# Performance work log

Measured on AMD Instinct MI355X. Metric: run time of the kernel, lower is better.

## Reference

```python
import jax, jax.numpy as jnp
import numpy as np

HEADS = 20  # SDXL-style: hidden_size 1280 / head_dim 64
IP_SCALE = 1.0


def setup_inputs() -> dict:
    key = jax.random.key(0)
    ks = jax.random.split(key, 12)
    B, Sq, T, C, D, NIP = 4, 4096, 77, 1280, 2048, 16
    s = lambda fan: 1.0 / np.sqrt(fan)
    # post-softmax multiplicative mask: col 0 (sot token) forced to 1, rest a binary spatial mask
    spat = (jax.random.uniform(ks[0], (1, Sq, 1)) < 0.5).astype(jnp.float32)
    attention_mask = jnp.concatenate([jnp.ones((1, Sq, 1)), jnp.tile(spat, (1, 1, T - 1))], axis=-1)
    return {
        "hidden_states": jax.random.normal(ks[1], (B, Sq, C), jnp.float32),
        "encoder_hidden_states": jax.random.normal(ks[2], (B, T, D), jnp.float32),
        "ip_hidden_states": jax.random.normal(ks[3], (B, NIP, D), jnp.float32),
        "attention_mask": attention_mask,
        "Wq": jax.random.normal(ks[4], (C, C), jnp.float32) * s(C),
        "Wk": jax.random.normal(ks[5], (D, C), jnp.float32) * s(D),
        "Wv": jax.random.normal(ks[6], (D, C), jnp.float32) * s(D),
        "Wo": jax.random.normal(ks[7], (C, C), jnp.float32) * s(C),
        "bo": jnp.zeros((C,), jnp.float32),
        "Wk_ip": jax.random.normal(ks[8], (D, C), jnp.float32) * s(D),
        "Wv_ip": jax.random.normal(ks[9], (D, C), jnp.float32) * s(D),
    }


def reference(hidden_states, encoder_hidden_states, ip_hidden_states, attention_mask,
              Wq, Wk, Wv, Wo, bo, Wk_ip, Wv_ip):
    B, Sq, C = hidden_states.shape
    H = HEADS
    d = C // H
    scale = d ** -0.5
    # projections (torch Linear with weights stored [in, out])
    q = (hidden_states @ Wq).reshape(B, Sq, H, d)
    k = (encoder_hidden_states @ Wk).reshape(B, -1, H, d)
    v = (encoder_hidden_states @ Wv).reshape(B, -1, H, d)
    # explicit QK^T softmax, then POST-softmax multiplicative mask (as in get_attention_scores + mask multiply)
    scores = jnp.einsum('bqhd,bkhd->bhqk', q, k) * scale
    probs = jax.nn.softmax(scores, axis=-1)
    probs = probs * attention_mask[:, None, :, :]  # [1,1,Sq,T] broadcast over batch*heads
    out = jnp.einsum('bhqk,bkhd->bqhd', probs, v).reshape(B, Sq, C)
    out = out @ Wo + bo  # to_out[0]; to_out[1] is dropout (identity at eval)
    # IP-adapter stream (single stream, no spatial ip mask): standard SDPA against ip tokens
    k_ip = (ip_hidden_states @ Wk_ip).reshape(B, -1, H, d)
    v_ip = (ip_hidden_states @ Wv_ip).reshape(B, -1, H, d)
    s_ip = jnp.einsum('bqhd,bkhd->bhqk', q, k_ip) * scale
    p_ip = jax.nn.softmax(s_ip, axis=-1)
    ip_out = jnp.einsum('bhqk,bkhd->bqhd', p_ip, v_ip).reshape(B, Sq, C)
    return out + IP_SCALE * ip_out
```

## Files before the change

kernel.cpp:

```cpp
#include <hip/hip_runtime.h>

typedef __attribute__((ext_vector_type(4))) float f32x4;
typedef __attribute__((ext_vector_type(8))) short s16x8;
typedef __attribute__((ext_vector_type(8))) __bf16 bf16x8;
typedef unsigned short u16;

__device__ __forceinline__ u16 f2b(float f) {
  union { float f; unsigned u; } x; x.f = f;
  unsigned r = x.u + 0x7fffu + ((x.u >> 16) & 1u);
  return (u16)(r >> 16);
}
__device__ __forceinline__ float b2f(u16 u) {
  union { unsigned u; float f; } x; x.u = ((unsigned)u) << 16;
  return x.f;
}
__device__ __forceinline__ void gld16(const void* g, void* l) {
  __builtin_amdgcn_global_load_lds(
      (const __attribute__((address_space(1))) unsigned int*)g,
      (__attribute__((address_space(3))) unsigned int*)l, 16, 0, 0);
}
__device__ __forceinline__ f32x4 mfma_bf16(s16x8 a, s16x8 b, f32x4 c) {
  return __builtin_amdgcn_mfma_f32_16x16x32_bf16(
      __builtin_bit_cast(bf16x8, a), __builtin_bit_cast(bf16x8, b), c, 0, 0, 0);
}

#define BAR() asm volatile("s_barrier" ::: "memory")
#define WAITVM4() asm volatile("s_waitcnt vmcnt(4)" ::: "memory")

__global__ void k_convert_all(const float* __restrict__ hs, const float* __restrict__ ehs,
                              const float* __restrict__ iph,
                              u16* __restrict__ hsb, u16* __restrict__ ehsb,
                              u16* __restrict__ ipb) {
  const int n1 = 16384 * 1280 / 4, n2 = 308 * 2048 / 4, n3 = 64 * 2048 / 4;
  int i = blockIdx.x * blockDim.x + threadIdx.x;
  const float* src; u16* dst; int j = i;
  if (i < n1) { src = hs; dst = hsb; }
  else if (i < n1 + n2) { src = ehs; dst = ehsb; j = i - n1; }
  else if (i < n1 + n2 + n3) { src = iph; dst = ipb; j = i - n1 - n2; }
  else return;
  float4 v = ((const float4*)src)[j];
  ushort4 o;
  o.x = f2b(v.x); o.y = f2b(v.y); o.z = f2b(v.z); o.w = f2b(v.w);
  ((ushort4*)dst)[j] = o;
}

__device__ __forceinline__ void transpose_tile(const float* __restrict__ W,
                                               u16* __restrict__ WT, int K, int N) {
  __shared__ float tile[32][33];
  int n0 = blockIdx.x * 32, k0 = blockIdx.y * 32;
  int tx = threadIdx.x & 31, ty = threadIdx.x >> 5;
#pragma unroll
  for (int i = 0; i < 32; i += 8)
    tile[ty + i][tx] = W[(size_t)(k0 + ty + i) * N + n0 + tx];
  __syncthreads();
#pragma unroll
  for (int i = 0; i < 32; i += 8)
    WT[(size_t)(n0 + ty + i) * K + k0 + tx] = f2b(tile[tx][ty + i]);
}

__global__ void k_transpose4(const float* W0, const float* W1, const float* W2,
                             const float* W3, u16* T0, u16* T1, u16* T2, u16* T3,
                             int K, int N) {
  int z = blockIdx.z;
  const float* W = (z == 0) ? W0 : (z == 1) ? W1 : (z == 2) ? W2 : W3;
  u16* T = (z == 0) ? T0 : (z == 1) ? T1 : (z == 2) ? T2 : T3;
  transpose_tile(W, T, K, N);
}
__global__ void k_transpose2(const float* W0, const float* W1, u16* T0, u16* T1,
                             int K, int N) {
  int z = blockIdx.z;
  transpose_tile(z ? W1 : W0, z ? T1 : T0, K, N);
}

__device__ __forceinline__ void gemm_core0(
    const u16* __restrict__ A, const u16* __restrict__ BT,
    int M, int N, int K, u16* __restrict__ outb, int m0, int n0) {
  const int tid = threadIdx.x;
  const int l = tid & 63;
  const int w = tid >> 6;
  const int wr = w >> 1, wc = w & 1;
  __shared__ u16 As[128 * 32];
  __shared__ u16 Bs[128 * 32];
  f32x4 acc[4][4] = {};

  const int o0 = tid * 16;
  const int o1 = o0 + 4096;
  const int ra0 = o0 >> 6, ca0 = (o0 & 63) >> 1;
  const int ra1 = o1 >> 6, ca1 = (o1 & 63) >> 1;
  int ga0 = m0 + ra0; if (ga0 >= M) ga0 = M - 1;
  int ga1 = m0 + ra1; if (ga1 >= M) ga1 = M - 1;
  const u16* Ar0 = A + (size_t)ga0 * K + ca0;
  const u16* Ar1 = A + (size_t)ga1 * K + ca1;
  const u16* Br0 = BT + (size_t)(n0 + ra0) * K + ca0;
  const u16* Br1 = BT + (size_t)(n0 + ra1) * K + ca1;

  for (int k0 = 0; k0 < K; k0 += 32) {
    gld16(Ar0 + k0, &As[o0 >> 1]);
    gld16(Ar1 + k0, &As[o1 >> 1]);
    gld16(Br0 + k0, &Bs[o0 >> 1]);
    gld16(Br1 + k0, &Bs[o1 >> 1]);
    __syncthreads();
    s16x8 af[4], bfr[4];
#pragma unroll
    for (int mi = 0; mi < 4; ++mi)
      af[mi] = *(const s16x8*)&As[(wr * 64 + mi * 16 + (l & 15)) * 32 + (l >> 4) * 8];
#pragma unroll
    for (int ni = 0; ni < 4; ++ni)
      bfr[ni] = *(const s16x8*)&Bs[(wc * 64 + ni * 16 + (l & 15)) * 32 + (l >> 4) * 8];
#pragma unroll
    for (int mi = 0; mi < 4; ++mi)
#pragma unroll
      for (int ni = 0; ni < 4; ++ni)
        acc[mi][ni] = mfma_bf16(af[mi], bfr[ni], acc[mi][ni]);
    __syncthreads();
  }

#pragma unroll
  for (int mi = 0; mi < 4; ++mi) {
    const int mbase = m0 + wr * 64 + mi * 16 + (l >> 4) * 4;
#pragma unroll
    for (int ni = 0; ni < 4; ++ni) {
      const int ncol = n0 + wc * 64 + ni * 16 + (l & 15);
#pragma unroll
      for (int r = 0; r < 4; ++r) {
        int m = mbase + r;
        if (m < M) outb[(size_t)m * N + ncol] = f2b(acc[mi][ni][r]);
      }
    }
  }
}

__global__ __launch_bounds__(256) void k_gemm_small4(
    const u16* __restrict__ ehsb, const u16* __restrict__ ipb,
    const u16* __restrict__ WkT, const u16* __restrict__ WvT,
    const u16* __restrict__ WkipT, const u16* __restrict__ WvipT,
    u16* kbuf, u16* vbuf, u16* kipb, u16* vipb) {
  const int z = blockIdx.z;
  const int M = (z < 2) ? 308 : 64;
  const int m0 = blockIdx.y * 128;
  if (m0 >= M) return;
  const u16* A = (z < 2) ? ehsb : ipb;
  const u16* BT = (z == 0) ? WkT : (z == 1) ? WvT : (z == 2) ? WkipT : WvipT;
  u16* out = (z == 0) ? kbuf : (z == 1) ? vbuf : (z == 2) ? kipb : vipb;
  gemm_core0(A, BT, M, 1280, 2048, out, m0, blockIdx.x * 128);
}

template <int EPI>
__global__ __launch_bounds__(512, 2) void k_gemm256(
    const u16* __restrict__ A, const u16* __restrict__ BT,
    int N, int K, float alpha,
    u16* __restrict__ outb, float* __restrict__ outf,
    const float* __restrict__ bias, const u16* __restrict__ ipadd,
    int nbx) {
  __shared__ u16 lds[65536];
  const int tid = threadIdx.x, l = tid & 63, w = tid >> 6;
  const int lr = l & 15, lg = l >> 4;
  const int wr = w >> 2, wc = w & 3;

  const int nwg = gridDim.x;
  const int q = nwg >> 3, r = nwg & 7;
  const int xcd = blockIdx.x & 7, lid = blockIdx.x >> 3;
  const int wg = (xcd < r) ? (xcd * (q + 1) + lid)
                           : (r * (q + 1) + (xcd - r) * q + lid);
  const int bm0 = (wg / nbx) * 256, bn0 = (wg % nbx) * 256;

  const int c0 = tid, c1 = tid + 512;
  const int row0 = c0 >> 2, row1 = c1 >> 2;
  const int sp0 = ((c0 & 3) ^ ((row0 >> 1) & 3)) * 8;
  const int sp1 = ((c1 & 3) ^ ((row1 >> 1) & 3)) * 8;
  const size_t aO0 = (size_t)(bm0 + row0) * K + sp0;
  const size_t aO1 = (size_t)(bm0 + row1) * K + sp1;
  const size_t bO0 = (size_t)(bn0 + row0) * K + sp0;
  const size_t bO1 = (size_t)(bn0 + row1) * K + sp1;
  const int d0 = c0 * 8, d1 = c1 * 8;

  const int KT = K >> 6;
  f32x4 acc[8][4] = {};
  s16x8 bfv[4], afv[4];

  const int xsw = (lg ^ ((lr >> 1) & 3)) * 8;
  const int aRow = (wr * 128 + lr) * 32 + xsw;
  const int bRow = 16384 + (wc * 64 + lr) * 32 + xsw;

#define STAGE_A(buf, kk, kt)                                            \
  {                                                                     \
    const int base_ = (buf) * 32768 + (kk) * 8192;                      \
    const size_t go_ = (size_t)(kt) * 64 + (kk) * 32;                   \
    gld16(A + aO0 + go_, &lds[base_ + d0]);                             \
    gld16(A + aO1 + go_, &lds[base_ + d1]);                             \
  }
#define STAGE_B(buf, kk, kt)                                            \
  {                                                                     \
    const int base_ = (buf) * 32768 + 16384 + (kk) * 8192;              \
    const size_t go_ = (size_t)(kt) * 64 + (kk) * 32;                   \
    gld16(BT + bO0 + go_, &lds[base_ + d0]);                            \
    gld16(BT + bO1 + go_, &lds[base_ + d1]);                            \
  }

  STAGE_A(0, 0, 0);
  STAGE_B(0, 0, 0);
  STAGE_A(0, 1, 0);
  STAGE_B(0, 1, 0);
  WAITVM4();
  BAR();

  int cur = 0;
  for (int j = 0; j < KT; ++j) {
    const int nx = cur ^ 1;
    const int cb = cur * 32768;
    const bool pf = (j + 1 < KT);
#pragma unroll
    for (int ni = 0; ni < 4; ++ni)
      bfv[ni] = *(const s16x8*)&lds[cb + bRow + ni * 512];
#pragma unroll
    for (int mi = 0; mi < 4; ++mi)
      afv[mi] = *(const s16x8*)&lds[cb + aRow + mi * 512];
    if (pf) STAGE_A(nx, 0, j + 1);
    __builtin_amdgcn_s_setprio(1);
#pragma unroll
    for (int mi = 0; mi < 4; ++mi)
#pragma unroll
      for (int ni = 0; ni < 4; ++ni)
        acc[mi][ni] = mfma_bf16(afv[mi], bfv[ni], acc[mi][ni]);
    __builtin_amdgcn_s_setprio(0);
    BAR();
#pragma unroll
    for (int mi = 0; mi < 4; ++mi)
      afv[mi] = *(const s16x8*)&lds[cb + aRow + (mi + 4) * 512];
    if (pf) STAGE_B(nx, 0, j + 1);
    __builtin_amdgcn_s_setprio(1);
#pragma unroll
    for (int mi = 0; mi < 4; ++mi)
#pragma unroll
      for (int ni = 0; ni < 4; ++ni)
        acc[mi + 4][ni] = mfma_bf16(afv[mi], bfv[ni], acc[mi + 4][ni]);
    __builtin_amdgcn_s_setprio(0);
    WAITVM4();
    BAR();
#pragma unroll
    for (int ni = 0; ni < 4; ++ni)
      bfv[ni] = *(const s16x8*)&lds[cb + 8192 + bRow + ni * 512];
#pragma unroll
    for (int mi = 0; mi < 4; ++mi)
      afv[mi] = *(const s16x8*)&lds[cb + 8192 + aRow + mi * 512];
    if (pf) STAGE_A(nx, 1, j + 1);
    __builtin_amdgcn_s_setprio(1);
#pragma unroll
    for (int mi = 0; mi < 4; ++mi)
#pragma unroll
      for (int ni = 0; ni < 4; ++ni)
        acc[mi][ni] = mfma_bf16(afv[mi], bfv[ni], acc[mi][ni]);
    __builtin_amdgcn_s_setprio(0);
    BAR();
#pragma unroll
    for (int mi = 0; mi < 4; ++mi)
      afv[mi] = *(const s16x8*)&lds[cb + 8192 + aRow + (mi + 4) * 512];
    if (pf) STAGE_B(nx, 1, j + 1);
    __builtin_amdgcn_s_setprio(1);
#pragma unroll
    for (int mi = 0; mi < 4; ++mi)
#pragma unroll
      for (int ni = 0; ni < 4; ++ni)
        acc[mi + 4][ni] = mfma_bf16(afv[mi], bfv[ni], acc[mi + 4][ni]);
    __builtin_amdgcn_s_setprio(0);
    WAITVM4();
    BAR();
    cur = nx;
  }

  asm volatile("s_waitcnt vmcnt(0)" ::: "memory");
  __syncthreads();

  if constexpr (EPI == 0) {
#pragma unroll
    for (int half = 0; half < 2; ++half) {
      if (half) __syncthreads();
      if (wr == half) {
#pragma unroll
        for (int mi = 0; mi < 8; ++mi) {
          const int row = mi * 16 + lg * 4;
#pragma unroll
          for (int ni = 0; ni < 4; ++ni) {
            const int col = wc * 64 + ni * 16 + lr;
#pragma unroll
            for (int rr = 0; rr < 4; ++rr)
              lds[(row + rr) * 256 + col] = f2b(acc[mi][ni][rr] * alpha);
          }
        }
      }
      __syncthreads();
      for (int s = tid; s < 4096; s += 512) {
        const int row = s >> 5, ch = s & 31;
        *(int4*)(outb + (size_t)(bm0 + half * 128 + row) * N + bn0 + ch * 8) =
            *(const int4*)&lds[row * 256 + ch * 8];
      }
    }
  } else {
#pragma unroll
    for (int mi = 0; mi < 8; ++mi) {
      const int mrow = bm0 + wr * 128 + mi * 16 + lg * 4;
#pragma unroll
      for (int ni = 0; ni < 4; ++ni) {
        const int ncol = bn0 + wc * 64 + ni * 16 + lr;
#pragma unroll
        for (int rr = 0; rr < 4; ++rr) {
          const size_t idx = (size_t)(mrow + rr) * N + ncol;
          outf[idx] = acc[mi][ni][rr] + bias[ncol] + b2f(ipadd[idx]);
        }
      }
    }
  }
#undef STAGE_A
#undef STAGE_B
}

__global__ __launch_bounds__(512, 4) void k_attn(
    const u16* __restrict__ Q,
    const u16* __restrict__ Kb,
    const u16* __restrict__ Vb,
    const u16* __restrict__ Kip,
    const u16* __restrict__ Vip,
    const float* __restrict__ mask,
    u16* __restrict__ Oattn,
    u16* __restrict__ Oip) {
  const int qt = blockIdx.x, h = blockIdx.y, b = blockIdx.z;
  const int tid = threadIdx.x, l = tid & 63, w = tid >> 6;
  const int lr = l & 15, lg = l >> 4;
  const int r0 = w * 16;
  const int m0 = b * 4096 + qt * 128;

  __shared__ u16 KV[192][72];
  __shared__ u16 Ps[128][104];
  __shared__ u16 P2s[128][40];

  const u16* qrow = Q + (size_t)(m0 + r0 + lr) * 1280 + h * 64;
  s16x8 aq0 = *(const s16x8*)(qrow + lg * 8);
  s16x8 aq1 = *(const s16x8*)(qrow + 32 + lg * 8);

  for (int s = tid; s < 192 * 8; s += 512) {
    const int row = s >> 3, seg = s & 7;
    int4 v = {0, 0, 0, 0};
    const u16* src = nullptr;
    if (row < 77)       src = Kb  + (size_t)(b * 77 + row) * 1280 + h * 64 + seg * 8;
    else if (row < 80)  src = nullptr;
    else if (row < 96)  src = Kip + (size_t)(b * 16 + row - 80) * 1280 + h * 64 + seg * 8;
    else if (row < 173) src = Vb  + (size_t)(b * 77 + row - 96) * 1280 + h * 64 + seg * 8;
    else if (row < 176) src = nullptr;
    else                src = Vip + (size_t)(b * 16 + row - 176) * 1280 + h * 64 + seg * 8;
    if (src) v = *(const int4*)src;
    *(int4*)&KV[row][(seg ^ ((row >> 3) & 3)) * 8] = v;
  }
  __syncthreads();

  f32x4 sc[5];
  f32x4 sip = {};
#pragma unroll
  for (int t5 = 0; t5 < 6; ++t5) {
    const int trow = t5 * 16 + lr;
    const int qz = (trow >> 3) & 3;
    s16x8 b0 = *(const s16x8*)&KV[trow][(lg ^ qz) * 8];
    s16x8 b1 = *(const s16x8*)&KV[trow][((lg + 4) ^ qz) * 8];
    f32x4 c = {};
    c = mfma_bf16(aq0, b0, c);
    c = mfma_bf16(aq1, b1, c);
    if (t5 < 5) sc[t5] = c; else sip = c;
  }

#pragma unroll
  for (int r = 0; r < 4; ++r) {
    float mx = fmaxf(fmaxf(fmaxf(sc[0][r], sc[1][r]), fmaxf(sc[2][r], sc[3][r])), sc[4][r]);
    mx = fmaxf(mx, __shfl_xor(mx, 1));
    mx = fmaxf(mx, __shfl_xor(mx, 2));
    mx = fmaxf(mx, __shfl_xor(mx, 4));
    mx = fmaxf(mx, __shfl_xor(mx, 8));
    float p[5], sm = 0.f;
#pragma unroll
    for (int t5 = 0; t5 < 5; ++t5) {
      bool valid = (t5 < 4) | (lr < 13);
      p[t5] = valid ? __expf(sc[t5][r] - mx) : 0.f;
      sm += p[t5];
    }
    sm += __shfl_xor(sm, 1);
    sm += __shfl_xor(sm, 2);
    sm += __shfl_xor(sm, 4);
    sm += __shfl_xor(sm, 8);
    const float inv = 1.0f / sm;
    const int row = r0 + lg * 4 + r;
    const int qg = qt * 128 + row;
#pragma unroll
    for (int t5 = 0; t5 < 5; ++t5) {
      int t = t5 * 16 + lr;
      float pf = 0.f;
      if (t < 77) pf = p[t5] * inv * mask[qg * 77 + t];
      Ps[row][t] = f2b(pf);
    }
    Ps[row][80 + lr] = 0;

    float m2 = sip[r];
    m2 = fmaxf(m2, __shfl_xor(m2, 1));
    m2 = fmaxf(m2, __shfl_xor(m2, 2));
    m2 = fmaxf(m2, __shfl_xor(m2, 4));
    m2 = fmaxf(m2, __shfl_xor(m2, 8));
    float pi = __expf(sip[r] - m2);
    float s2 = pi;
    s2 += __shfl_xor(s2, 1);
    s2 += __shfl_xor(s2, 2);
    s2 += __shfl_xor(s2, 4);
    s2 += __shfl_xor(s2, 8);
    P2s[row][lr] = 0;
    P2s[row][16 + lr] = f2b(pi / s2);
  }

  s16x8 ap[3];
#pragma unroll
  for (int ks = 0; ks < 3; ++ks)
    ap[ks] = *(const s16x8*)&Ps[r0 + lr][ks * 32 + lg * 8];
  s16x8 aip = *(const s16x8*)&P2s[r0 + lr][lg * 8];

  f32x4 om[4], oi[4];
#pragma unroll
  for (int nt = 0; nt < 4; ++nt) {
    const int dcol = (nt * 16 + lr) ^ (lg << 3);
    f32x4 o = {};
#pragma unroll
    for (int ks = 0; ks < 3; ++ks) {
      s16x8 bv;
#pragma unroll
      for (int j = 0; j < 8; ++j)
        bv[j] = (short)KV[96 + ks * 32 + lg * 8 + j][dcol];
      o = mfma_bf16(ap[ks], bv, o);
    }
    s16x8 bip;
#pragma unroll
    for (int j = 0; j < 8; ++j)
      bip[j] = (short)KV[160 + lg * 8 + j][dcol];
    f32x4 o2 = {};
    o2 = mfma_bf16(aip, bip, o2);
    om[nt] = o;
    oi[nt] = o2;
  }

  __syncthreads();

  u16 (*Om)[72] = (u16(*)[72]) & KV[0][0];
  u16 (*Oi)[72] = (u16(*)[72]) & Ps[0][0];
#pragma unroll
  for (int nt = 0; nt < 4; ++nt)
#pragma unroll
    for (int r = 0; r < 4; ++r) {
      const int row = r0 + lg * 4 + r;
      const int d = nt * 16 + lr;
      Om[row][d] = f2b(om[nt][r]);
      Oi[row][d] = f2b(oi[nt][r]);
    }
  __syncthreads();

  for (int s = tid; s < 128 * 8; s += 512) {
    const int row = s >> 3, seg = s & 7;
    const size_t g = (size_t)(m0 + row) * 1280 + h * 64 + seg * 8;
    *(int4*)(Oattn + g) = *(const int4*)&Om[row][seg * 8];
    *(int4*)(Oip + g) = *(const int4*)&Oi[row][seg * 8];
  }
}

extern "C" void kernel_launch(void* const* d_in, const int* in_sizes, int n_in,
                              void* d_out, int out_size, void* d_ws, size_t ws_size,
                              hipStream_t stream) {
  (void)in_sizes; (void)n_in; (void)out_size; (void)ws_size;
  const float* hs   = (const float*)d_in[0];
  const float* ehs  = (const float*)d_in[1];
  const float* iph  = (const float*)d_in[2];
  const float* mask = (const float*)d_in[3];
  const float* Wq   = (const float*)d_in[4];
  const float* Wk   = (const float*)d_in[5];
  const float* Wv   = (const float*)d_in[6];
  const float* Wo   = (const float*)d_in[7];
  const float* bo   = (const float*)d_in[8];
  const float* Wkip = (const float*)d_in[9];
  const float* Wvip = (const float*)d_in[10];
  float* out = (float*)d_out;

  char* ws = (char*)d_ws;
  size_t off = 0;
  auto alloc = [&](size_t bytes) {
    char* p = ws + off;
    off += (bytes + 255) & ~(size_t)255;
    return p;
  };
  u16* hsb   = (u16*)alloc(16384ull * 1280 * 2);
  u16* qbuf  = (u16*)alloc(16384ull * 1280 * 2);
  u16* ipout = (u16*)alloc(16384ull * 1280 * 2);
  u16* WqT   = (u16*)alloc(1280ull * 1280 * 2);
  u16* WoT   = (u16*)alloc(1280ull * 1280 * 2);
  u16* WkT   = (u16*)alloc(1280ull * 2048 * 2);
  u16* WvT   = (u16*)alloc(1280ull * 2048 * 2);
  u16* WkipT = (u16*)alloc(1280ull * 2048 * 2);
  u16* WvipT = (u16*)alloc(1280ull * 2048 * 2);
  u16* ehsb  = (u16*)alloc(308ull * 2048 * 2);
  u16* ipb   = (u16*)alloc(64ull * 2048 * 2);
  u16* kbuf  = (u16*)alloc(308ull * 1280 * 2);
  u16* vbuf  = (u16*)alloc(308ull * 1280 * 2);
  u16* kipb  = (u16*)alloc(64ull * 1280 * 2);
  u16* vipb  = (u16*)alloc(64ull * 1280 * 2);

  const int ntot4 = (16384 * 1280 + 308 * 2048 + 64 * 2048) / 4;
  k_convert_all<<<(ntot4 + 255) / 256, 256, 0, stream>>>(hs, ehs, iph, hsb, ehsb, ipb);
  k_transpose4<<<dim3(40, 64, 4), 256, 0, stream>>>(Wk, Wv, Wkip, Wvip,
                                                    WkT, WvT, WkipT, WvipT, 2048, 1280);
  k_transpose2<<<dim3(40, 40, 2), 256, 0, stream>>>(Wq, Wo, WqT, WoT, 1280, 1280);

  k_gemm256<0><<<320, 512, 0, stream>>>(hsb, WqT, 1280, 1280, 0.125f,
                                        qbuf, nullptr, nullptr, nullptr, 5);
  k_gemm_small4<<<dim3(10, 3, 4), 256, 0, stream>>>(ehsb, ipb, WkT, WvT, WkipT, WvipT,
                                                    kbuf, vbuf, kipb, vipb);

  k_attn<<<dim3(32, 20, 4), 512, 0, stream>>>(qbuf, kbuf, vbuf, kipb, vipb, mask,
                                              hsb, ipout);

  k_gemm256<1><<<320, 512, 0, stream>>>(hsb, WoT, 1280, 1280, 1.f,
                                        nullptr, out, bo, ipout, 5);
}
```

Measured before the change: 308.5 us.

## Widen projection GEMM tile to 256x320 so grid fits one wave

Changes the Q and output projection GEMM tile from 256x256 to 256x320, giving 256 workgroups that exactly cover the CUs in a single wave instead of 320 workgroups with a tail. B staging adds a third load issued only by the first four waves, with matching per-wave vmcnt waits. LDS grows to 144 KB and launch bounds drop to one block per CU, trading co-residency latency hiding for removal of wave quantization and higher per-wave MFMA reuse.

```diff
diff --git a/kernel.cpp b/kernel.cpp
--- a/kernel.cpp
+++ b/kernel.cpp
@@ -25,7 +25,6 @@
 }
 
 #define BAR() asm volatile("s_barrier" ::: "memory")
-#define WAITVM4() asm volatile("s_waitcnt vmcnt(4)" ::: "memory")
 
 __global__ void k_convert_all(const float* __restrict__ hs, const float* __restrict__ ehs,
                               const float* __restrict__ iph,
@@ -146,129 +145,137 @@
 }
 
 template <int EPI>
-__global__ __launch_bounds__(512, 2) void k_gemm256(
+__global__ __launch_bounds__(512, 1) void k_gemm256(
     const u16* __restrict__ A, const u16* __restrict__ BT,
     int N, int K, float alpha,
     u16* __restrict__ outb, float* __restrict__ outf,
     const float* __restrict__ bias, const u16* __restrict__ ipadd,
     int nbx) {
-  __shared__ u16 lds[65536];
+  __shared__ u16 lds[73728];
   const int tid = threadIdx.x, l = tid & 63, w = tid >> 6;
   const int lr = l & 15, lg = l >> 4;
   const int wr = w >> 2, wc = w & 3;
+  const bool wlo = (w < 4);
 
   const int nwg = gridDim.x;
   const int q = nwg >> 3, r = nwg & 7;
   const int xcd = blockIdx.x & 7, lid = blockIdx.x >> 3;
   const int wg = (xcd < r) ? (xcd * (q + 1) + lid)
                            : (r * (q + 1) + (xcd - r) * q + lid);
-  const int bm0 = (wg / nbx) * 256, bn0 = (wg % nbx) * 256;
-
-  const int c0 = tid, c1 = tid + 512;
-  const int row0 = c0 >> 2, row1 = c1 >> 2;
-  const int sp0 = ((c0 & 3) ^ ((row0 >> 1) & 3)) * 8;
-  const int sp1 = ((c1 & 3) ^ ((row1 >> 1) & 3)) * 8;
-  const size_t aO0 = (size_t)(bm0 + row0) * K + sp0;
-  const size_t aO1 = (size_t)(bm0 + row1) * K + sp1;
-  const size_t bO0 = (size_t)(bn0 + row0) * K + sp0;
-  const size_t bO1 = (size_t)(bn0 + row1) * K + sp1;
-  const int d0 = c0 * 8, d1 = c1 * 8;
+  const int bm0 = (wg / nbx) * 256, bn0 = (wg % nbx) * 320;
+
+  const int srow = tid >> 2;
+  const int sslot = ((tid & 3) ^ ((srow >> 1) & 3)) * 8;
+  const size_t aO0 = (size_t)(bm0 + srow) * K + sslot;
+  const size_t aO1 = aO0 + (size_t)128 * K;
+  const size_t bO0 = (size_t)(bn0 + srow) * K + sslot;
+  const size_t bO1 = bO0 + (size_t)128 * K;
+  const size_t bO2 = bO0 + (size_t)256 * K;
+  const int d0 = tid * 8, d1 = (tid + 512) * 8, d2 = (tid + 1024) * 8;
 
   const int KT = K >> 6;
-  f32x4 acc[8][4] = {};
-  s16x8 bfv[4], afv[4];
+  f32x4 acc[8][5] = {};
+  s16x8 bfv[5], afv[4];
 
   const int xsw = (lg ^ ((lr >> 1) & 3)) * 8;
   const int aRow = (wr * 128 + lr) * 32 + xsw;
-  const int bRow = 16384 + (wc * 64 + lr) * 32 + xsw;
-
-#define STAGE_A(buf, kk, kt)                                            \
-  {                                                                     \
-    const int base_ = (buf) * 32768 + (kk) * 8192;                      \
-    const size_t go_ = (size_t)(kt) * 64 + (kk) * 32;                   \
-    gld16(A + aO0 + go_, &lds[base_ + d0]);                             \
-    gld16(A + aO1 + go_, &lds[base_ + d1]);                             \
-  }
-#define STAGE_B(buf, kk, kt)                                            \
-  {                                                                     \
-    const int base_ = (buf) * 32768 + 16384 + (kk) * 8192;              \
-    const size_t go_ = (size_t)(kt) * 64 + (kk) * 32;                   \
-    gld16(BT + bO0 + go_, &lds[base_ + d0]);                            \
-    gld16(BT + bO1 + go_, &lds[base_ + d1]);                            \
-  }
+  const int bRow = 32768 + (wc * 80 + lr) * 32 + xsw;
+
+#define STAGE_A(buf, kk, kt)                                           \
+  {                                                                    \
+    const int base_ = (buf) * 16384 + (kk) * 8192;                     \
+    const size_t go_ = (size_t)(kt) * 64 + (kk) * 32;                  \
+    gld16(A + aO0 + go_, &lds[base_ + d0]);                            \
+    gld16(A + aO1 + go_, &lds[base_ + d1]);                            \
+  }
+#define STAGE_B(buf, kk, kt)                                           \
+  {                                                                    \
+    const int base_ = 32768 + (buf) * 20480 + (kk) * 10240;            \
+    const size_t go_ = (size_t)(kt) * 64 + (kk) * 32;                  \
+    gld16(BT + bO0 + go_, &lds[base_ + d0]);                           \
+    gld16(BT + bO1 + go_, &lds[base_ + d1]);                           \
+    if (wlo) gld16(BT + bO2 + go_, &lds[base_ + d2]);                  \
+  }
+#define WAITVM()                                                       \
+  {                                                                    \
+    if (wlo) asm volatile("s_waitcnt vmcnt(5)" ::: "memory");          \
+    else     asm volatile("s_waitcnt vmcnt(4)" ::: "memory");          \
+  }
+#define WAITVM0() asm volatile("s_waitcnt vmcnt(0)" ::: "memory")
 
   STAGE_A(0, 0, 0);
   STAGE_B(0, 0, 0);
   STAGE_A(0, 1, 0);
   STAGE_B(0, 1, 0);
-  WAITVM4();
+  WAITVM();
   BAR();
 
   int cur = 0;
   for (int j = 0; j < KT; ++j) {
     const int nx = cur ^ 1;
-    const int cb = cur * 32768;
+    const int ab = cur * 16384;
+    const int bb = cur * 20480;
     const bool pf = (j + 1 < KT);
 #pragma unroll
-    for (int ni = 0; ni < 4; ++ni)
-      bfv[ni] = *(const s16x8*)&lds[cb + bRow + ni * 512];
-#pragma unroll
-    for (int mi = 0; mi < 4; ++mi)
-      afv[mi] = *(const s16x8*)&lds[cb + aRow + mi * 512];
+    for (int ni = 0; ni < 5; ++ni)
+      bfv[ni] = *(const s16x8*)&lds[bb + bRow + ni * 512];
+#pragma unroll
+    for (int mi = 0; mi < 4; ++mi)
+      afv[mi] = *(const s16x8*)&lds[ab + aRow + mi * 512];
     if (pf) STAGE_A(nx, 0, j + 1);
     __builtin_amdgcn_s_setprio(1);
 #pragma unroll
     for (int mi = 0; mi < 4; ++mi)
 #pragma unroll
-      for (int ni = 0; ni < 4; ++ni)
+      for (int ni = 0; ni < 5; ++ni)
         acc[mi][ni] = mfma_bf16(afv[mi], bfv[ni], acc[mi][ni]);
     __builtin_amdgcn_s_setprio(0);
     BAR();
 #pragma unroll
     for (int mi = 0; mi < 4; ++mi)
-      afv[mi] = *(const s16x8*)&lds[cb + aRow + (mi + 4) * 512];
+      afv[mi] = *(const s16x8*)&lds[ab + aRow + (mi + 4) * 512];
     if (pf) STAGE_B(nx, 0, j + 1);
     __builtin_amdgcn_s_setprio(1);
 #pragma unroll
     for (int mi = 0; mi < 4; ++mi)
 #pragma unroll
-      for (int ni = 0; ni < 4; ++ni)
+      for (int ni = 0; ni < 5; ++ni)
         acc[mi + 4][ni] = mfma_bf16(afv[mi], bfv[ni], acc[mi + 4][ni]);
     __builtin_amdgcn_s_setprio(0);
-    WAITVM4();
+    if (pf) { WAITVM(); } else { WAITVM0(); }
     BAR();
 #pragma unroll
-    for (int ni = 0; ni < 4; ++ni)
-      bfv[ni] = *(const s16x8*)&lds[cb + 8192 + bRow + ni * 512];
-#pragma unroll
-    for (int mi = 0; mi < 4; ++mi)
-      afv[mi] = *(const s16x8*)&lds[cb + 8192 + aRow + mi * 512];
+    for (int ni = 0; ni < 5; ++ni)
+      bfv[ni] = *(const s16x8*)&lds[bb + 10240 + bRow + ni * 512];
+#pragma unroll
+    for (int mi = 0; mi < 4; ++mi)
+      afv[mi] = *(const s16x8*)&lds[ab + 8192 + aRow + mi * 512];
     if (pf) STAGE_A(nx, 1, j + 1);
     __builtin_amdgcn_s_setprio(1);
 #pragma unroll
     for (int mi = 0; mi < 4; ++mi)
 #pragma unroll
-      for (int ni = 0; ni < 4; ++ni)
+      for (int ni = 0; ni < 5; ++ni)
         acc[mi][ni] = mfma_bf16(afv[mi], bfv[ni], acc[mi][ni]);
     __builtin_amdgcn_s_setprio(0);
     BAR();
 #pragma unroll
     for (int mi = 0; mi < 4; ++mi)
-      afv[mi] = *(const s16x8*)&lds[cb + 8192 + aRow + (mi + 4) * 512];
+      afv[mi] = *(const s16x8*)&lds[ab + 8192 + aRow + (mi + 4) * 512];
     if (pf) STAGE_B(nx, 1, j + 1);
     __builtin_amdgcn_s_setprio(1);
 #pragma unroll
     for (int mi = 0; mi < 4; ++mi)
 #pragma unroll
-      for (int ni = 0; ni < 4; ++ni)
+      for (int ni = 0; ni < 5; ++ni)
         acc[mi + 4][ni] = mfma_bf16(afv[mi], bfv[ni], acc[mi + 4][ni]);
     __builtin_amdgcn_s_setprio(0);
-    WAITVM4();
+    if (pf) { WAITVM(); } else { WAITVM0(); }
     BAR();
     cur = nx;
   }
 
-  asm volatile("s_waitcnt vmcnt(0)" ::: "memory");
+  WAITVM0();
   __syncthreads();
 
   if constexpr (EPI == 0) {
@@ -280,19 +287,21 @@
         for (int mi = 0; mi < 8; ++mi) {
           const int row = mi * 16 + lg * 4;
 #pragma unroll
-          for (int ni = 0; ni < 4; ++ni) {
-            const int col = wc * 64 + ni * 16 + lr;
+          for (int ni = 0; ni < 5; ++ni) {
+            const int col = wc * 80 + ni * 16 + lr;
 #pragma unroll
             for (int rr = 0; rr < 4; ++rr)
-              lds[(row + rr) * 256 + col] = f2b(acc[mi][ni][rr] * alpha);
+              lds[(row + rr) * 320 + col] = f2b(acc[mi][ni][rr] * alpha);
           }
         }
       }
       __syncthreads();
-      for (int s = tid; s < 4096; s += 512) {
-        const int row = s >> 5, ch = s & 31;
-        *(int4*)(outb + (size_t)(bm0 + half * 128 + row) * N + bn0 + ch * 8) =
-            *(const int4*)&lds[row * 256 + ch * 8];
+      const int rrow = tid >> 2;
+#pragma unroll
+      for (int jj = 0; jj < 10; ++jj) {
+        const int ch = (tid & 3) + jj * 4;
+        *(int4*)(outb + (size_t)(bm0 + half * 128 + rrow) * N + bn0 + ch * 8) =
+            *(const int4*)&lds[rrow * 320 + ch * 8];
       }
     }
   } else {
@@ -300,8 +309,8 @@
     for (int mi = 0; mi < 8; ++mi) {
       const int mrow = bm0 + wr * 128 + mi * 16 + lg * 4;
 #pragma unroll
-      for (int ni = 0; ni < 4; ++ni) {
-        const int ncol = bn0 + wc * 64 + ni * 16 + lr;
+      for (int ni = 0; ni < 5; ++ni) {
+        const int ncol = bn0 + wc * 80 + ni * 16 + lr;
 #pragma unroll
         for (int rr = 0; rr < 4; ++rr) {
           const size_t idx = (size_t)(mrow + rr) * N + ncol;
@@ -312,6 +321,8 @@
   }
 #undef STAGE_A
 #undef STAGE_B
+#undef WAITVM
+#undef WAITVM0
 }
 
 __global__ __launch_bounds__(512, 4) void k_attn(
@@ -509,14 +520,14 @@
                                                     WkT, WvT, WkipT, WvipT, 2048, 1280);
   k_transpose2<<<dim3(40, 40, 2), 256, 0, stream>>>(Wq, Wo, WqT, WoT, 1280, 1280);
 
-  k_gemm256<0><<<320, 512, 0, stream>>>(hsb, WqT, 1280, 1280, 0.125f,
-                                        qbuf, nullptr, nullptr, nullptr, 5);
+  k_gemm256<0><<<256, 512, 0, stream>>>(hsb, WqT, 1280, 1280, 0.125f,
+                                        qbuf, nullptr, nullptr, nullptr, 4);
   k_gemm_small4<<<dim3(10, 3, 4), 256, 0, stream>>>(ehsb, ipb, WkT, WvT, WkipT, WvipT,
                                                     kbuf, vbuf, kipb, vipb);
 
   k_attn<<<dim3(32, 20, 4), 512, 0, stream>>>(qbuf, kbuf, vbuf, kipb, vipb, mask,
                                               hsb, ipout);
 
-  k_gemm256<1><<<320, 512, 0, stream>>>(hsb, WoT, 1280, 1280, 1.f,
-                                        nullptr, out, bo, ipout, 5);
-}
+  k_gemm256<1><<<256, 512, 0, stream>>>(hsb, WoT, 1280, 1280, 1.f,
+                                        nullptr, out, bo, ipout, 4);
+}
```

Result: faster. 266.3 us (-13.7%).
